# Optimization experiments

Measured on AMD Instinct MI355X. Metric: run time of the kernel, lower is better.

Reference implementation:

```python
import jax, jax.numpy as jnp
import numpy as np

N, NF, DIM, H, DH, DEPTH, EDIM, NB = 256, 127, 128, 8, 64, 6, 3, 512
INNER = H * DH  # 512
SCALE = DH ** -0.5
EPS = 1e-5


def setup_inputs() -> dict:
    key = jax.random.key(0)
    ks = jax.random.split(key, 16)
    p = lambda k, shape: jax.random.normal(k, shape, jnp.float32) * 0.02
    return {
        "coordinates": jax.random.normal(ks[0], (N, 3), jnp.float32),
        "bonds": jax.random.randint(ks[1], (NB, 2), 0, N),
        "noise_level": jax.random.uniform(ks[2], (1,), jnp.float32),
        "atom_emb": p(ks[3], (N, NF)),
        "ln1_g": jnp.ones((DEPTH, DIM)), "ln1_b": jnp.zeros((DEPTH, DIM)),
        "Wq": p(ks[4], (DEPTH, DIM, INNER)), "bq": jnp.zeros((DEPTH, INNER)),
        "Wkv": p(ks[5], (DEPTH, DIM, 2 * INNER)), "bkv": jnp.zeros((DEPTH, 2 * INNER)),
        "We": p(ks[6], (DEPTH, EDIM, INNER)), "be": jnp.zeros((DEPTH, INNER)),
        "Wo": p(ks[7], (DEPTH, INNER, DIM)), "bo": jnp.zeros((DEPTH, DIM)),
        "Wg1": p(ks[8], (DEPTH, 3 * DIM)),
        "ln2_g": jnp.ones((DEPTH, DIM)), "ln2_b": jnp.zeros((DEPTH, DIM)),
        "W1": p(ks[9], (DEPTH, DIM, 4 * DIM)), "b1": jnp.zeros((DEPTH, 4 * DIM)),
        "W2": p(ks[10], (DEPTH, 4 * DIM, DIM)), "b2": jnp.zeros((DEPTH, DIM)),
        "Wg2": p(ks[11], (DEPTH, 3 * DIM)),
        "out_w": p(ks[12], (DIM, 1)), "out_b": jnp.zeros((1,)),
    }


def _layernorm(x, g, b):
    m = jnp.mean(x, axis=-1, keepdims=True)
    v = jnp.mean((x - m) ** 2, axis=-1, keepdims=True)
    return (x - m) * jax.lax.rsqrt(v + EPS) * g + b


def _gated_residual(x, res, Wg):
    # Linear(3*dim -> 1, no bias) then sigmoid; mask is all-True so no masking.
    gate = jax.nn.sigmoid(jnp.concatenate([x, res, x - res], axis=-1) @ Wg)[..., None]
    return x * gate + res * (1.0 - gate)


def _forward(coordinates, bonds, noise_level, atom_emb, ln1_g, ln1_b, Wq, bq,
             Wkv, bkv, We, be, Wo, bo, Wg1, ln2_g, ln2_b, W1, b1, W2, b2, Wg2,
             out_w, out_b):
    n = coordinates.shape[0]
    # nodes: [n, NF] atom embeddings (looked up at arange(n)) + noise column -> [n, DIM]
    noise_col = jnp.broadcast_to(noise_level.reshape(1, 1), (n, 1))
    nodes = jnp.concatenate([atom_emb, noise_col], axis=-1)
    # dense edge tensor [n, n, 3]: coordinate differences at bonded pairs, antisymmetric
    bi, bj = bonds[:, 0], bonds[:, 1]
    diff = coordinates[bi] - coordinates[bj]
    edges = jnp.zeros((n, n, EDIM), jnp.float32).at[bi, bj].set(diff).at[bj, bi].set(-diff)

    for l in range(DEPTH):
        # --- edge-biased multi-head attention (PreNorm) ---
        x = _layernorm(nodes, ln1_g[l], ln1_b[l])
        q = (x @ Wq[l] + bq[l]).reshape(n, H, DH).transpose(1, 0, 2)          # [h, i, d]
        kv = x @ Wkv[l] + bkv[l]
        k = kv[:, :INNER].reshape(n, H, DH).transpose(1, 0, 2)                # [h, j, d]
        v = kv[:, INNER:].reshape(n, H, DH).transpose(1, 0, 2)                # [h, j, d]
        e = (edges @ We[l] + be[l]).reshape(n, n, H, DH).transpose(2, 0, 1, 3)  # [h, i, j, d]
        k_ij = k[:, None, :, :] + e                                            # [h, i, j, d]
        v_ij = v[:, None, :, :] + e
        sim = jnp.einsum('hid,hijd->hij', q, k_ij) * SCALE
        attn = jax.nn.softmax(sim, axis=-1)  # mask is all ones -> no-op
        out = jnp.einsum('hij,hijd->hid', attn, v_ij)                          # [h, i, d]
        out = out.transpose(1, 0, 2).reshape(n, INNER) @ Wo[l] + bo[l]         # [n, DIM]
        nodes = _gated_residual(out, nodes, Wg1[l])
        # --- feedforward (PreNorm) + gated residual ---
        y = _layernorm(nodes, ln2_g[l], ln2_b[l])
        y = jax.nn.gelu(y @ W1[l] + b1[l], approximate=False) @ W2[l] + b2[l]
        nodes = _gated_residual(y, nodes, Wg2[l])

    energy = nodes @ out_w + out_b  # [n, 1]
    return energy[None, :, :]       # [1, n, 1]


def reference(coordinates, bonds, noise_level, atom_emb, ln1_g, ln1_b, Wq, bq,
              Wkv, bkv, We, be, Wo, bo, Wg1, ln2_g, ln2_b, W1, b1, W2, b2, Wg2,
              out_w, out_b):
    return _forward(coordinates, bonds, noise_level, atom_emb, ln1_g, ln1_b,
                    Wq, bq, Wkv, bkv, We, be, Wo, bo, Wg1, ln2_g, ln2_b,
                    W1, b1, W2, b2, Wg2, out_w, out_b)
```

## Files before the change

kernel.cpp:

```cpp
#include <hip/hip_runtime.h>

#define NN     256
#define NF     127
#define DIM    128
#define NH     8
#define DH     64
#define INNER  512
#define DEPTH  6
#define NB     512
#define ATTN_SCALE 0.125f
#define LN_EPS 1e-5f

#define FMA4(A_, S_, V_) { A_.x=fmaf(S_,(V_).x,A_.x); A_.y=fmaf(S_,(V_).y,A_.y); \
                           A_.z=fmaf(S_,(V_).z,A_.z); A_.w=fmaf(S_,(V_).w,A_.w); }

__device__ __forceinline__ float wred_sum(float v){
#pragma unroll
  for(int o=32;o;o>>=1) v += __shfl_xor(v,o);
  return v;
}
__device__ __forceinline__ float wred_max(float v){
#pragma unroll
  for(int o=32;o;o>>=1) v = fmaxf(v,__shfl_xor(v,o));
  return v;
}
__device__ __forceinline__ float2 wred_sum2(float a, float b){
#pragma unroll
  for(int o=32;o;o>>=1){ a += __shfl_xor(a,o); b += __shfl_xor(b,o); }
  return make_float2(a,b);
}

__device__ __forceinline__ void ln_wave(float n0, float n1,
                                        const float* g, const float* b, int l,
                                        float& x0, float& x1){
  float2 sv = wred_sum2(n0+n1, n0*n0+n1*n1);
  float m  = sv.x*(1.f/DIM);
  float var = sv.y*(1.f/DIM) - m*m;
  float rs = rsqrtf(var + LN_EPS);
  x0 = (n0-m)*rs*g[l]    + b[l];
  x1 = (n1-m)*rs*g[64+l] + b[64+l];
}

__device__ __forceinline__ void gate_wave(float o0, float o1, float& n0, float& n1,
                                          const float* Wg, int l){
  float gv = o0*Wg[l]    + n0*Wg[DIM+l]    + (o0-n0)*Wg[2*DIM+l]
           + o1*Wg[64+l] + n1*Wg[DIM+64+l] + (o1-n1)*Wg[2*DIM+64+l];
  gv = wred_sum(gv);
  float gate = 1.f/(1.f + expf(-gv));
  n0 = o0*gate + n0*(1.f-gate);
  n1 = o1*gate + n1*(1.f-gate);
}

__device__ __forceinline__ void mvp128_512(const float* xin, const float* W,
                                           float* SC, int t){
  const int cg4 = (t&127)<<2, fq = t>>7;
  float4 acc = make_float4(0.f,0.f,0.f,0.f);
#pragma unroll 8
  for(int f=fq*32; f<fq*32+32; f++){
    float4 wv = *(const float4*)(W + f*INNER + cg4);
    float xv = xin[f];
    FMA4(acc, xv, wv);
  }
  *(float4*)(SC + fq*INNER + cg4) = acc;
}

__device__ __forceinline__ void mvp128_1024(const float* xin, const float* W,
                                            float* SC, int t){
  const int cg4 = (t&255)<<2, rh = t>>8;
  float4 acc = make_float4(0.f,0.f,0.f,0.f);
#pragma unroll 8
  for(int f=rh*64; f<rh*64+64; f++){
    float4 wv = *(const float4*)(W + f*(2*INNER) + cg4);
    float xv = xin[f];
    FMA4(acc, xv, wv);
  }
  *(float4*)(SC + rh*(2*INNER) + cg4) = acc;
}

__device__ __forceinline__ void mvp512_128(const float* ain, const float* W,
                                           float* SC, int t){
  const int cg4 = (t&31)<<2, fg = t>>5;
  float4 acc = make_float4(0.f,0.f,0.f,0.f);
#pragma unroll 8
  for(int f=fg*32; f<fg*32+32; f++){
    float4 wv = *(const float4*)(W + f*DIM + cg4);
    float av = ain[f];
    FMA4(acc, av, wv);
  }
  *(float4*)(SC + fg*DIM + cg4) = acc;
}

__device__ __forceinline__ void qkv_tail(const float* xs, int i,
    const float* Wq, const float* bq, const float* Wkv, const float* bkv,
    const float* be, float* qgn, float* kTn, float* vgn, float* SC, int t){
  mvp128_512(xs, Wq, SC, t);
  __syncthreads();
  qgn[i*INNER + t] = bq[t] + SC[t] + SC[INNER+t] + SC[2*INNER+t] + SC[3*INNER+t];
  __syncthreads();
  mvp128_1024(xs, Wkv, SC, t);
  __syncthreads();
#pragma unroll
  for(int cc=0; cc<2; cc++){
    int c = t + cc*512;
    float s = bkv[c] + SC[c] + SC[2*INNER+c];
    if(c < INNER) kTn[c*NN + i]            = s + be[c];
    else          vgn[i*INNER + c - INNER] = s + be[c-INNER];
  }
}

__global__ __launch_bounds__(512) void k_qkv0(const float* atom_emb, const float* noise,
    float* nodes, const float* ln1_g, const float* ln1_b,
    const float* Wq, const float* bq, const float* Wkv, const float* bkv, const float* be,
    float* qg, float* kT, float* vg){
  __shared__ __align__(16) float SC[2048];
  __shared__ __align__(16) float xsm[DIM];
  const int t = threadIdx.x, i = blockIdx.x;
  const int w = t>>6, l = t&63;
  float nd0 = (l<NF)?      atom_emb[i*NF + l]      : noise[0];
  float nd1 = (64+l<NF)?   atom_emb[i*NF + 64 + l] : noise[0];
  if(w==0){ nodes[i*DIM + l] = nd0; nodes[i*DIM + 64 + l] = nd1; }
  float x0, x1;
  ln_wave(nd0, nd1, ln1_g, ln1_b, l, x0, x1);
  xsm[l] = x0; xsm[64+l] = x1;
  __syncthreads();
  qkv_tail(xsm, i, Wq, bq, Wkv, bkv, be, qg, kT, vg, SC, t);
}

__global__ __launch_bounds__(512) void k_layer(
    float* nodes, const float* qg, const float* kT, const float* vg,
    float* qg_n, float* kT_n, float* vg_n,
    const int* bonds, const float* coords,
    const float* We,
    const float* Wo, const float* bo, const float* Wg1,
    const float* ln2_g, const float* ln2_b,
    const float* W1, const float* b1, const float* W2, const float* b2,
    const float* Wg2,
    const float* ln1_g_n, const float* ln1_b_n,
    const float* Wq_n, const float* bq_n, const float* Wkv_n, const float* bkv_n,
    const float* be_n,
    const float* out_w, const float* out_b, float* eout, int has_next)
{
  __shared__ __align__(16) float SC[2048];
  __shared__ __align__(16) float qs[INNER];
  __shared__ __align__(16) float ao[INNER];
  __shared__ __align__(16) float eb[3*NN];
  __shared__ __align__(16) float xsm[DIM];
  const int t = threadIdx.x, i = blockIdx.x;
  const int w = t>>6, l = t&63;

  qs[t] = qg[i*INNER + t];
  eb[t&511] = 0.f;
  if(t < 256) eb[512 + t] = 0.f;
  float nd0 = nodes[i*DIM + l];
  float nd1 = nodes[i*DIM + 64 + l];
  __syncthreads();

  {
    const int bi = bonds[2*t], bj = bonds[2*t+1];
    if(bi==i || bj==i){
      float dx = coords[3*bi+0] - coords[3*bj+0];
      float dy = coords[3*bi+1] - coords[3*bj+1];
      float dz = coords[3*bi+2] - coords[3*bj+2];
      if(bi==i){ eb[bj]=dx;  eb[NN+bj]=dy;  eb[2*NN+bj]=dz;  }
      if(bj==i){ eb[bi]=-dx; eb[NN+bi]=-dy; eb[2*NN+bi]=-dz; }
    }
  }
  __syncthreads();

  {
    const int h = w, j0 = l<<2, qb = h*DH;
    float qwe0, qwe1, qwe2;
    {
      float qv = qs[qb + l];
      qwe0 = qv*We[0*INNER + qb + l];
      qwe1 = qv*We[1*INNER + qb + l];
      qwe2 = qv*We[2*INNER + qb + l];
#pragma unroll
      for(int o=32;o;o>>=1){
        qwe0 += __shfl_xor(qwe0,o); qwe1 += __shfl_xor(qwe1,o); qwe2 += __shfl_xor(qwe2,o);
      }
    }
    const float* kTh = kT + qb*NN;
    float s0=0.f,s1=0.f,s2=0.f,s3=0.f;
#pragma unroll 8
    for(int o=0;o<DH;o++){
      float qv = qs[qb + o];
      float4 kk = *(const float4*)(kTh + o*NN + j0);
      s0=fmaf(qv,kk.x,s0); s1=fmaf(qv,kk.y,s1); s2=fmaf(qv,kk.z,s2); s3=fmaf(qv,kk.w,s3);
    }
    float4 ex = *(const float4*)(eb + j0);
    float4 ey = *(const float4*)(eb + NN + j0);
    float4 ez = *(const float4*)(eb + 2*NN + j0);
    s0 = (s0 + qwe0*ex.x + qwe1*ey.x + qwe2*ez.x)*ATTN_SCALE;
    s1 = (s1 + qwe0*ex.y + qwe1*ey.y + qwe2*ez.y)*ATTN_SCALE;
    s2 = (s2 + qwe0*ex.z + qwe1*ey.z + qwe2*ez.z)*ATTN_SCALE;
    s3 = (s3 + qwe0*ex.w + qwe1*ey.w + qwe2*ez.w)*ATTN_SCALE;
    float mx = wred_max(fmaxf(fmaxf(s0,s1),fmaxf(s2,s3)));
    float p0=expf(s0-mx), p1=expf(s1-mx), p2=expf(s2-mx), p3=expf(s3-mx);
    float inv = 1.f / wred_sum(p0+p1+p2+p3);
    float a0=p0*inv, a1=p1*inv, a2=p2*inv, a3=p3*inv;
    *(float4*)(SC + h*NN + j0) = make_float4(a0,a1,a2,a3);
    float c0 = a0*ex.x + a1*ex.y + a2*ex.z + a3*ex.w;
    float c1 = a0*ey.x + a1*ey.y + a2*ey.z + a3*ey.w;
    float c2 = a0*ez.x + a1*ez.y + a2*ez.z + a3*ez.w;
    c0 = wred_sum(c0); c1 = wred_sum(c1); c2 = wred_sum(c2);
    __builtin_amdgcn_wave_barrier();
    const int dq = (l&15)<<2, jg = l>>4;
    const float* vb = vg + qb + dq;
    float4 acc = make_float4(0.f,0.f,0.f,0.f);
#pragma unroll 8
    for(int jj=0;jj<64;jj++){
      int j = (jg<<6) + ((jj + (jg<<3)) & 63);
      float a = SC[h*NN + j];
      float4 vv = *(const float4*)(vb + j*INNER);
      FMA4(acc, a, vv);
    }
#pragma unroll
    for(int o=16;o<64;o<<=1){
      acc.x += __shfl_xor(acc.x,o); acc.y += __shfl_xor(acc.y,o);
      acc.z += __shfl_xor(acc.z,o); acc.w += __shfl_xor(acc.w,o);
    }
    if(l<16){
      float4 we0 = *(const float4*)(We + 0*INNER + qb + dq);
      float4 we1 = *(const float4*)(We + 1*INNER + qb + dq);
      float4 we2 = *(const float4*)(We + 2*INNER + qb + dq);
      float4 ov;
      ov.x = acc.x + c0*we0.x + c1*we1.x + c2*we2.x;
      ov.y = acc.y + c0*we0.y + c1*we1.y + c2*we2.y;
      ov.z = acc.z + c0*we0.z + c1*we1.z + c2*we2.z;
      ov.w = acc.w + c0*we0.w + c1*we1.w + c2*we2.w;
      *(float4*)(ao + qb + dq) = ov;
    }
  }
  __syncthreads();

  mvp512_128(ao, Wo, SC, t);
  __syncthreads();
  {
    float o0 = bo[l], o1 = bo[64+l];
#pragma unroll
    for(int fg=0; fg<16; fg++){ o0 += SC[fg*DIM + l]; o1 += SC[fg*DIM + 64 + l]; }
    gate_wave(o0, o1, nd0, nd1, Wg1, l);
    float x0, x1;
    ln_wave(nd0, nd1, ln2_g, ln2_b, l, x0, x1);
    xsm[l] = x0; xsm[64+l] = x1;
  }
  __syncthreads();

  mvp128_512(xsm, W1, SC, t);
  __syncthreads();
  {
    float a = b1[t] + SC[t] + SC[INNER+t] + SC[2*INNER+t] + SC[3*INNER+t];
    qs[t] = 0.5f*a*(1.f + erff(a*0.70710678118654752440f));
  }
  __syncthreads();
  mvp512_128(qs, W2, SC, t);
  __syncthreads();
  {
    float y0 = b2[l], y1 = b2[64+l];
#pragma unroll
    for(int fg=0; fg<16; fg++){ y0 += SC[fg*DIM + l]; y1 += SC[fg*DIM + 64 + l]; }
    gate_wave(y0, y1, nd0, nd1, Wg2, l);
    if(w==0){ nodes[i*DIM + l] = nd0; nodes[i*DIM + 64 + l] = nd1; }
    if(has_next){
      float x0, x1;
      ln_wave(nd0, nd1, ln1_g_n, ln1_b_n, l, x0, x1);
      xsm[l] = x0; xsm[64+l] = x1;
    } else if(w==0){
      float ev = nd0*out_w[l] + nd1*out_w[64+l];
      ev = wred_sum(ev);
      if(l==0) eout[i] = ev + out_b[0];
    }
  }
  if(has_next){
    __syncthreads();
    qkv_tail(xsm, i, Wq_n, bq_n, Wkv_n, bkv_n, be_n, qg_n, kT_n, vg_n, SC, t);
  }
}

extern "C" void kernel_launch(void* const* d_in, const int* in_sizes, int n_in,
                              void* d_out, int out_size, void* d_ws, size_t ws_size,
                              hipStream_t stream){
  const float* coords   = (const float*)d_in[0];
  const int*   bonds    = (const int*  )d_in[1];
  const float* noise    = (const float*)d_in[2];
  const float* atom_emb = (const float*)d_in[3];
  const float* ln1_g = (const float*)d_in[4];
  const float* ln1_b = (const float*)d_in[5];
  const float* Wq    = (const float*)d_in[6];
  const float* bq    = (const float*)d_in[7];
  const float* Wkv   = (const float*)d_in[8];
  const float* bkv   = (const float*)d_in[9];
  const float* We    = (const float*)d_in[10];
  const float* be    = (const float*)d_in[11];
  const float* Wo    = (const float*)d_in[12];
  const float* bo    = (const float*)d_in[13];
  const float* Wg1   = (const float*)d_in[14];
  const float* ln2_g = (const float*)d_in[15];
  const float* ln2_b = (const float*)d_in[16];
  const float* W1    = (const float*)d_in[17];
  const float* b1    = (const float*)d_in[18];
  const float* W2    = (const float*)d_in[19];
  const float* b2    = (const float*)d_in[20];
  const float* Wg2   = (const float*)d_in[21];
  const float* out_w = (const float*)d_in[22];
  const float* out_b = (const float*)d_in[23];

  float* ws = (float*)d_ws;
  float* nodes   = ws;
  float* qbuf[2] = { ws +  32768, ws + 163840 };
  float* kbuf[2] = { ws + 294912, ws + 425984 };
  float* vbuf[2] = { ws + 557056, ws + 688128 };

  k_qkv0<<<NN, 512, 0, stream>>>(atom_emb, noise, nodes, ln1_g, ln1_b,
                                 Wq, bq, Wkv, bkv, be,
                                 qbuf[0], kbuf[0], vbuf[0]);
  for(int l=0; l<DEPTH; l++){
    int cur = l&1, nxt = cur^1;
    int has_next = (l < DEPTH-1);
    int ln = has_next ? l+1 : l;
    k_layer<<<NN, 512, 0, stream>>>(
      nodes, qbuf[cur], kbuf[cur], vbuf[cur],
      qbuf[nxt], kbuf[nxt], vbuf[nxt],
      bonds, coords,
      We  + (size_t)l*3*INNER,
      Wo  + (size_t)l*INNER*DIM, bo + (size_t)l*DIM, Wg1 + (size_t)l*3*DIM,
      ln2_g + (size_t)l*DIM, ln2_b + (size_t)l*DIM,
      W1  + (size_t)l*DIM*4*DIM, b1 + (size_t)l*4*DIM,
      W2  + (size_t)l*4*DIM*DIM, b2 + (size_t)l*DIM, Wg2 + (size_t)l*3*DIM,
      ln1_g + (size_t)ln*DIM, ln1_b + (size_t)ln*DIM,
      Wq  + (size_t)ln*DIM*INNER, bq + (size_t)ln*INNER,
      Wkv + (size_t)ln*DIM*2*INNER, bkv + (size_t)ln*2*INNER,
      be  + (size_t)ln*INNER,
      out_w, out_b, (float*)d_out, has_next);
  }
}
```

Baseline: 304.9 us.

## Double block size to 1024 threads and split attention across two waves per head

Measured after the change: 322.2 us. +5.7%, slower.

```diff
diff --git a/kernel.cpp b/kernel.cpp
--- a/kernel.cpp
+++ b/kernel.cpp
@@ -8,6 +8,7 @@
 #define INNER  512
 #define DEPTH  6
 #define NB     512
+#define TB     1024
 #define ATTN_SCALE 0.125f
 #define LN_EPS 1e-5f
 
@@ -53,36 +54,34 @@
 
 __device__ __forceinline__ void mvp128_512(const float* xin, const float* W,
                                            float* SC, int t){
-  const int cg4 = (t&127)<<2, fq = t>>7;
+  const int cg4 = (t&127)<<2, fo = t>>7;
   float4 acc = make_float4(0.f,0.f,0.f,0.f);
-#pragma unroll 8
-  for(int f=fq*32; f<fq*32+32; f++){
+#pragma unroll
+  for(int f=fo*16; f<fo*16+16; f++){
     float4 wv = *(const float4*)(W + f*INNER + cg4);
     float xv = xin[f];
     FMA4(acc, xv, wv);
   }
-  *(float4*)(SC + fq*INNER + cg4) = acc;
-}
-
+  *(float4*)(SC + fo*INNER + cg4) = acc;
+}
 __device__ __forceinline__ void mvp128_1024(const float* xin, const float* W,
                                             float* SC, int t){
-  const int cg4 = (t&255)<<2, rh = t>>8;
+  const int cg4 = (t&255)<<2, fq = t>>8;
   float4 acc = make_float4(0.f,0.f,0.f,0.f);
-#pragma unroll 8
-  for(int f=rh*64; f<rh*64+64; f++){
+#pragma unroll
+  for(int f=fq*32; f<fq*32+32; f++){
     float4 wv = *(const float4*)(W + f*(2*INNER) + cg4);
     float xv = xin[f];
     FMA4(acc, xv, wv);
   }
-  *(float4*)(SC + rh*(2*INNER) + cg4) = acc;
-}
-
+  *(float4*)(SC + fq*(2*INNER) + cg4) = acc;
+}
 __device__ __forceinline__ void mvp512_128(const float* ain, const float* W,
                                            float* SC, int t){
   const int cg4 = (t&31)<<2, fg = t>>5;
   float4 acc = make_float4(0.f,0.f,0.f,0.f);
-#pragma unroll 8
-  for(int f=fg*32; f<fg*32+32; f++){
+#pragma unroll
+  for(int f=fg*16; f<fg*16+16; f++){
     float4 wv = *(const float4*)(W + f*DIM + cg4);
     float av = ain[f];
     FMA4(acc, av, wv);
@@ -95,29 +94,35 @@
     const float* be, float* qgn, float* kTn, float* vgn, float* SC, int t){
   mvp128_512(xs, Wq, SC, t);
   __syncthreads();
-  qgn[i*INNER + t] = bq[t] + SC[t] + SC[INNER+t] + SC[2*INNER+t] + SC[3*INNER+t];
+  if(t < INNER){
+    float s = bq[t];
+#pragma unroll
+    for(int fo=0; fo<8; fo++) s += SC[fo*INNER + t];
+    qgn[i*INNER + t] = s;
+  }
   __syncthreads();
   mvp128_1024(xs, Wkv, SC, t);
   __syncthreads();
-#pragma unroll
-  for(int cc=0; cc<2; cc++){
-    int c = t + cc*512;
-    float s = bkv[c] + SC[c] + SC[2*INNER+c];
+  {
+    int c = t;
+    float s = bkv[c];
+#pragma unroll
+    for(int fq=0; fq<4; fq++) s += SC[fq*(2*INNER) + c];
     if(c < INNER) kTn[c*NN + i]            = s + be[c];
     else          vgn[i*INNER + c - INNER] = s + be[c-INNER];
   }
 }
 
-__global__ __launch_bounds__(512) void k_qkv0(const float* atom_emb, const float* noise,
+__global__ __launch_bounds__(TB) void k_qkv0(const float* atom_emb, const float* noise,
     float* nodes, const float* ln1_g, const float* ln1_b,
     const float* Wq, const float* bq, const float* Wkv, const float* bkv, const float* be,
     float* qg, float* kT, float* vg){
-  __shared__ __align__(16) float SC[2048];
+  __shared__ __align__(16) float SC[4096];
   __shared__ __align__(16) float xsm[DIM];
   const int t = threadIdx.x, i = blockIdx.x;
   const int w = t>>6, l = t&63;
-  float nd0 = (l<NF)?      atom_emb[i*NF + l]      : noise[0];
-  float nd1 = (64+l<NF)?   atom_emb[i*NF + 64 + l] : noise[0];
+  float nd0 = (l<NF)?    atom_emb[i*NF + l]      : noise[0];
+  float nd1 = (64+l<NF)? atom_emb[i*NF + 64 + l] : noise[0];
   if(w==0){ nodes[i*DIM + l] = nd0; nodes[i*DIM + 64 + l] = nd1; }
   float x0, x1;
   ln_wave(nd0, nd1, ln1_g, ln1_b, l, x0, x1);
@@ -126,7 +131,7 @@
   qkv_tail(xsm, i, Wq, bq, Wkv, bkv, be, qg, kT, vg, SC, t);
 }
 
-__global__ __launch_bounds__(512) void k_layer(
+__global__ __launch_bounds__(TB) void k_layer(
     float* nodes, const float* qg, const float* kT, const float* vg,
     float* qg_n, float* kT_n, float* vg_n,
     const int* bonds, const float* coords,
@@ -140,22 +145,25 @@
     const float* be_n,
     const float* out_w, const float* out_b, float* eout, int has_next)
 {
-  __shared__ __align__(16) float SC[2048];
+  __shared__ __align__(16) float SC[4096];
+  __shared__ __align__(16) float aW[NH*NN];
+  __shared__ __align__(16) float aoP[2*NH*DH];
+  __shared__ __align__(16) float cEs[NH*3];
   __shared__ __align__(16) float qs[INNER];
   __shared__ __align__(16) float ao[INNER];
   __shared__ __align__(16) float eb[3*NN];
   __shared__ __align__(16) float xsm[DIM];
+  __shared__ __align__(16) float o128[DIM];
   const int t = threadIdx.x, i = blockIdx.x;
   const int w = t>>6, l = t&63;
 
-  qs[t] = qg[i*INNER + t];
-  eb[t&511] = 0.f;
-  if(t < 256) eb[512 + t] = 0.f;
+  if(t < INNER) qs[t] = qg[i*INNER + t];
+  if(t < 3*NN)  eb[t] = 0.f;
   float nd0 = nodes[i*DIM + l];
   float nd1 = nodes[i*DIM + 64 + l];
   __syncthreads();
 
-  {
+  if(t < NB){
     const int bi = bonds[2*t], bj = bonds[2*t+1];
     if(bi==i || bj==i){
       float dx = coords[3*bi+0] - coords[3*bj+0];
@@ -168,7 +176,7 @@
   __syncthreads();
 
   {
-    const int h = w, j0 = l<<2, qb = h*DH;
+    const int h = w>>1, half = w&1, j0 = l<<2, qb = h*DH;
     float qwe0, qwe1, qwe2;
     {
       float qv = qs[qb + l];
@@ -182,36 +190,41 @@
     }
     const float* kTh = kT + qb*NN;
     float s0=0.f,s1=0.f,s2=0.f,s3=0.f;
-#pragma unroll 8
-    for(int o=0;o<DH;o++){
+#pragma unroll
+    for(int o=half*32; o<half*32+32; o++){
       float qv = qs[qb + o];
       float4 kk = *(const float4*)(kTh + o*NN + j0);
       s0=fmaf(qv,kk.x,s0); s1=fmaf(qv,kk.y,s1); s2=fmaf(qv,kk.z,s2); s3=fmaf(qv,kk.w,s3);
     }
+    *(float4*)(SC + (half*NH + h)*NN + j0) = make_float4(s0,s1,s2,s3);
+    __syncthreads();
+    float4 pA = *(const float4*)(SC + h*NN + j0);
+    float4 pB = *(const float4*)(SC + (NH+h)*NN + j0);
     float4 ex = *(const float4*)(eb + j0);
     float4 ey = *(const float4*)(eb + NN + j0);
     float4 ez = *(const float4*)(eb + 2*NN + j0);
-    s0 = (s0 + qwe0*ex.x + qwe1*ey.x + qwe2*ez.x)*ATTN_SCALE;
-    s1 = (s1 + qwe0*ex.y + qwe1*ey.y + qwe2*ez.y)*ATTN_SCALE;
-    s2 = (s2 + qwe0*ex.z + qwe1*ey.z + qwe2*ez.z)*ATTN_SCALE;
-    s3 = (s3 + qwe0*ex.w + qwe1*ey.w + qwe2*ez.w)*ATTN_SCALE;
+    s0 = (pA.x+pB.x + qwe0*ex.x + qwe1*ey.x + qwe2*ez.x)*ATTN_SCALE;
+    s1 = (pA.y+pB.y + qwe0*ex.y + qwe1*ey.y + qwe2*ez.y)*ATTN_SCALE;
+    s2 = (pA.z+pB.z + qwe0*ex.z + qwe1*ey.z + qwe2*ez.z)*ATTN_SCALE;
+    s3 = (pA.w+pB.w + qwe0*ex.w + qwe1*ey.w + qwe2*ez.w)*ATTN_SCALE;
     float mx = wred_max(fmaxf(fmaxf(s0,s1),fmaxf(s2,s3)));
     float p0=expf(s0-mx), p1=expf(s1-mx), p2=expf(s2-mx), p3=expf(s3-mx);
     float inv = 1.f / wred_sum(p0+p1+p2+p3);
     float a0=p0*inv, a1=p1*inv, a2=p2*inv, a3=p3*inv;
-    *(float4*)(SC + h*NN + j0) = make_float4(a0,a1,a2,a3);
+    if(half==0) *(float4*)(aW + h*NN + j0) = make_float4(a0,a1,a2,a3);
     float c0 = a0*ex.x + a1*ex.y + a2*ex.z + a3*ex.w;
     float c1 = a0*ey.x + a1*ey.y + a2*ey.z + a3*ey.w;
     float c2 = a0*ez.x + a1*ez.y + a2*ez.z + a3*ez.w;
     c0 = wred_sum(c0); c1 = wred_sum(c1); c2 = wred_sum(c2);
-    __builtin_amdgcn_wave_barrier();
+    if(half==0 && l==0){ cEs[h*3+0]=c0; cEs[h*3+1]=c1; cEs[h*3+2]=c2; }
+    __syncthreads();
     const int dq = (l&15)<<2, jg = l>>4;
     const float* vb = vg + qb + dq;
     float4 acc = make_float4(0.f,0.f,0.f,0.f);
-#pragma unroll 8
-    for(int jj=0;jj<64;jj++){
-      int j = (jg<<6) + ((jj + (jg<<3)) & 63);
-      float a = SC[h*NN + j];
+#pragma unroll
+    for(int jj=0;jj<32;jj++){
+      int j = half*128 + (jg<<5) + ((jj + (jg<<3)) & 31);
+      float a = aW[h*NN + j];
       float4 vv = *(const float4*)(vb + j*INNER);
       FMA4(acc, a, vv);
     }
@@ -220,26 +233,28 @@
       acc.x += __shfl_xor(acc.x,o); acc.y += __shfl_xor(acc.y,o);
       acc.z += __shfl_xor(acc.z,o); acc.w += __shfl_xor(acc.w,o);
     }
-    if(l<16){
-      float4 we0 = *(const float4*)(We + 0*INNER + qb + dq);
-      float4 we1 = *(const float4*)(We + 1*INNER + qb + dq);
-      float4 we2 = *(const float4*)(We + 2*INNER + qb + dq);
-      float4 ov;
-      ov.x = acc.x + c0*we0.x + c1*we1.x + c2*we2.x;
-      ov.y = acc.y + c0*we0.y + c1*we1.y + c2*we2.y;
-      ov.z = acc.z + c0*we0.z + c1*we1.z + c2*we2.z;
-      ov.w = acc.w + c0*we0.w + c1*we1.w + c2*we2.w;
-      *(float4*)(ao + qb + dq) = ov;
-    }
+    if(l<16) *(float4*)(aoP + (half*NH + h)*DH + dq) = acc;
+  }
+  __syncthreads();
+  if(t < INNER){
+    const int c = t, h2 = c>>6, d = c&63;
+    ao[c] = aoP[h2*DH + d] + aoP[(NH+h2)*DH + d]
+          + cEs[h2*3+0]*We[0*INNER+c] + cEs[h2*3+1]*We[1*INNER+c]
+          + cEs[h2*3+2]*We[2*INNER+c];
   }
   __syncthreads();
 
   mvp512_128(ao, Wo, SC, t);
   __syncthreads();
+  if(t < DIM){
+    float s = bo[t];
+#pragma unroll
+    for(int fg=0; fg<32; fg++) s += SC[fg*DIM + t];
+    o128[t] = s;
+  }
+  __syncthreads();
   {
-    float o0 = bo[l], o1 = bo[64+l];
-#pragma unroll
-    for(int fg=0; fg<16; fg++){ o0 += SC[fg*DIM + l]; o1 += SC[fg*DIM + 64 + l]; }
+    float o0 = o128[l], o1 = o128[64+l];
     gate_wave(o0, o1, nd0, nd1, Wg1, l);
     float x0, x1;
     ln_wave(nd0, nd1, ln2_g, ln2_b, l, x0, x1);
@@ -249,17 +264,24 @@
 
   mvp128_512(xsm, W1, SC, t);
   __syncthreads();
+  if(t < INNER){
+    float a = b1[t];
+#pragma unroll
+    for(int fo=0; fo<8; fo++) a += SC[fo*INNER + t];
+    qs[t] = 0.5f*a*(1.f + erff(a*0.70710678118654752440f));
+  }
+  __syncthreads();
+  mvp512_128(qs, W2, SC, t);
+  __syncthreads();
+  if(t < DIM){
+    float s = b2[t];
+#pragma unroll
+    for(int fg=0; fg<32; fg++) s += SC[fg*DIM + t];
+    o128[t] = s;
+  }
+  __syncthreads();
   {
-    float a = b1[t] + SC[t] + SC[INNER+t] + SC[2*INNER+t] + SC[3*INNER+t];
-    qs[t] = 0.5f*a*(1.f + erff(a*0.70710678118654752440f));
-  }
-  __syncthreads();
-  mvp512_128(qs, W2, SC, t);
-  __syncthreads();
-  {
-    float y0 = b2[l], y1 = b2[64+l];
-#pragma unroll
-    for(int fg=0; fg<16; fg++){ y0 += SC[fg*DIM + l]; y1 += SC[fg*DIM + 64 + l]; }
+    float y0 = o128[l], y1 = o128[64+l];
     gate_wave(y0, y1, nd0, nd1, Wg2, l);
     if(w==0){ nodes[i*DIM + l] = nd0; nodes[i*DIM + 64 + l] = nd1; }
     if(has_next){
@@ -274,7 +296,8 @@
   }
   if(has_next){
     __syncthreads();
-    qkv_tail(xsm, i, Wq_n, bq_n, Wkv_n, bkv_n, be_n, qg_n, kT_n, vg_n, SC, t);
+    qkv_tail(xsm, i, Wq_n, bq_n, Wkv_n, bkv_n, be_n,
+             qg_n, kT_n, vg_n, SC, t);
   }
 }
 
@@ -312,14 +335,14 @@
   float* kbuf[2] = { ws + 294912, ws + 425984 };
   float* vbuf[2] = { ws + 557056, ws + 688128 };
 
-  k_qkv0<<<NN, 512, 0, stream>>>(atom_emb, noise, nodes, ln1_g, ln1_b,
-                                 Wq, bq, Wkv, bkv, be,
-                                 qbuf[0], kbuf[0], vbuf[0]);
+  k_qkv0<<<NN, TB, 0, stream>>>(atom_emb, noise, nodes, ln1_g, ln1_b,
+                                Wq, bq, Wkv, bkv, be,
+                                qbuf[0], kbuf[0], vbuf[0]);
   for(int l=0; l<DEPTH; l++){
     int cur = l&1, nxt = cur^1;
     int has_next = (l < DEPTH-1);
     int ln = has_next ? l+1 : l;
-    k_layer<<<NN, 512, 0, stream>>>(
+    k_layer<<<NN, TB, 0, stream>>>(
       nodes, qbuf[cur], kbuf[cur], vbuf[cur],
       qbuf[nxt], kbuf[nxt], vbuf[nxt],
       bonds, coords,
```

## Split attention into separate head-major kernel grouping eight queries per block

Applied to the files above, without the earlier changes.

Result: no change. 303.6 us (-0.4%).

```diff
diff --git a/kernel.cpp b/kernel.cpp
--- a/kernel.cpp
+++ b/kernel.cpp
@@ -63,7 +63,6 @@
   }
   *(float4*)(SC + fq*INNER + cg4) = acc;
 }
-
 __device__ __forceinline__ void mvp128_1024(const float* xin, const float* W,
                                             float* SC, int t){
   const int cg4 = (t&255)<<2, rh = t>>8;
@@ -76,7 +75,6 @@
   }
   *(float4*)(SC + rh*(2*INNER) + cg4) = acc;
 }
-
 __device__ __forceinline__ void mvp512_128(const float* ain, const float* W,
                                            float* SC, int t){
   const int cg4 = (t&31)<<2, fg = t>>5;
@@ -116,8 +114,8 @@
   __shared__ __align__(16) float xsm[DIM];
   const int t = threadIdx.x, i = blockIdx.x;
   const int w = t>>6, l = t&63;
-  float nd0 = (l<NF)?      atom_emb[i*NF + l]      : noise[0];
-  float nd1 = (64+l<NF)?   atom_emb[i*NF + 64 + l] : noise[0];
+  float nd0 = (l<NF)?    atom_emb[i*NF + l]      : noise[0];
+  float nd1 = (64+l<NF)? atom_emb[i*NF + 64 + l] : noise[0];
   if(w==0){ nodes[i*DIM + l] = nd0; nodes[i*DIM + 64 + l] = nd1; }
   float x0, x1;
   ln_wave(nd0, nd1, ln1_g, ln1_b, l, x0, x1);
@@ -126,11 +124,105 @@
   qkv_tail(xsm, i, Wq, bq, Wkv, bkv, be, qg, kT, vg, SC, t);
 }
 
+__global__ __launch_bounds__(512) void k_attn(
+    const float* qg, const float* kT, const float* vg,
+    const int* bonds, const float* coords, const float* We,
+    float* aog)
+{
+  __shared__ __align__(16) float qsm[8*DH];
+  __shared__ __align__(16) float eb[8][3*NN];
+  __shared__ __align__(16) float aW[8][NN];
+  const int t = threadIdx.x;
+  const int h = blockIdx.x >> 5, i0 = (blockIdx.x & 31) << 3;
+  const int w = t>>6, l = t&63;
+  const int qb = h*DH, j0 = l<<2;
+
+  qsm[w*DH + l] = qg[(i0+w)*INNER + qb + l];
+#pragma unroll
+  for(int cc=0; cc<12; cc++) (&eb[0][0])[cc*512 + t] = 0.f;
+  __syncthreads();
+
+  {
+    const int bi = bonds[2*t], bj = bonds[2*t+1];
+    const bool hi = (bi>=i0 && bi<i0+8), hj = (bj>=i0 && bj<i0+8);
+    if(hi || hj){
+      float dx = coords[3*bi+0] - coords[3*bj+0];
+      float dy = coords[3*bi+1] - coords[3*bj+1];
+      float dz = coords[3*bi+2] - coords[3*bj+2];
+      if(hi){ float* e = eb[bi-i0]; e[bj]=dx;  e[NN+bj]=dy;  e[2*NN+bj]=dz;  }
+      if(hj){ float* e = eb[bj-i0]; e[bi]=-dx; e[NN+bi]=-dy; e[2*NN+bi]=-dz; }
+    }
+  }
+  __syncthreads();
+
+  float qwe0, qwe1, qwe2;
+  {
+    float qv = qsm[w*DH + l];
+    qwe0 = qv*We[0*INNER + qb + l];
+    qwe1 = qv*We[1*INNER + qb + l];
+    qwe2 = qv*We[2*INNER + qb + l];
+#pragma unroll
+    for(int o=32;o;o>>=1){
+      qwe0 += __shfl_xor(qwe0,o); qwe1 += __shfl_xor(qwe1,o); qwe2 += __shfl_xor(qwe2,o);
+    }
+  }
+  const float* kTh = kT + qb*NN;
+  float s0=0.f,s1=0.f,s2=0.f,s3=0.f;
+#pragma unroll 8
+  for(int o=0;o<DH;o++){
+    float qv = qsm[w*DH + o];
+    float4 kk = *(const float4*)(kTh + o*NN + j0);
+    s0=fmaf(qv,kk.x,s0); s1=fmaf(qv,kk.y,s1); s2=fmaf(qv,kk.z,s2); s3=fmaf(qv,kk.w,s3);
+  }
+  const float* e = eb[w];
+  float4 ex = *(const float4*)(e + j0);
+  float4 ey = *(const float4*)(e + NN + j0);
+  float4 ez = *(const float4*)(e + 2*NN + j0);
+  s0 = (s0 + qwe0*ex.x + qwe1*ey.x + qwe2*ez.x)*ATTN_SCALE;
+  s1 = (s1 + qwe0*ex.y + qwe1*ey.y + qwe2*ez.y)*ATTN_SCALE;
+  s2 = (s2 + qwe0*ex.z + qwe1*ey.z + qwe2*ez.z)*ATTN_SCALE;
+  s3 = (s3 + qwe0*ex.w + qwe1*ey.w + qwe2*ez.w)*ATTN_SCALE;
+  float mx = wred_max(fmaxf(fmaxf(s0,s1),fmaxf(s2,s3)));
+  float p0=expf(s0-mx), p1=expf(s1-mx), p2=expf(s2-mx), p3=expf(s3-mx);
+  float inv = 1.f / wred_sum(p0+p1+p2+p3);
+  float a0=p0*inv, a1=p1*inv, a2=p2*inv, a3=p3*inv;
+  *(float4*)(aW[w] + j0) = make_float4(a0,a1,a2,a3);
+  float c0 = a0*ex.x + a1*ex.y + a2*ex.z + a3*ex.w;
+  float c1 = a0*ey.x + a1*ey.y + a2*ey.z + a3*ey.w;
+  float c2 = a0*ez.x + a1*ez.y + a2*ez.z + a3*ez.w;
+  c0 = wred_sum(c0); c1 = wred_sum(c1); c2 = wred_sum(c2);
+  __builtin_amdgcn_wave_barrier();
+  const int dq = (l&15)<<2, jg = l>>4;
+  const float* vb = vg + qb + dq;
+  float4 acc = make_float4(0.f,0.f,0.f,0.f);
+#pragma unroll 8
+  for(int jj=0;jj<64;jj++){
+    int j = (jg<<6) + ((jj + (jg<<3)) & 63);
+    float a = aW[w][j];
+    float4 vv = *(const float4*)(vb + j*INNER);
+    FMA4(acc, a, vv);
+  }
+#pragma unroll
+  for(int o=16;o<64;o<<=1){
+    acc.x += __shfl_xor(acc.x,o); acc.y += __shfl_xor(acc.y,o);
+    acc.z += __shfl_xor(acc.z,o); acc.w += __shfl_xor(acc.w,o);
+  }
+  if(l<16){
+    float4 we0 = *(const float4*)(We + 0*INNER + qb + dq);
+    float4 we1 = *(const float4*)(We + 1*INNER + qb + dq);
+    float4 we2 = *(const float4*)(We + 2*INNER + qb + dq);
+    float4 ov;
+    ov.x = acc.x + c0*we0.x + c1*we1.x + c2*we2.x;
+    ov.y = acc.y + c0*we0.y + c1*we1.y + c2*we2.y;
+    ov.z = acc.z + c0*we0.z + c1*we1.z + c2*we2.z;
+    ov.w = acc.w + c0*we0.w + c1*we1.w + c2*we2.w;
+    *(float4*)(aog + (i0+w)*INNER + qb + dq) = ov;
+  }
+}
+
 __global__ __launch_bounds__(512) void k_layer(
-    float* nodes, const float* qg, const float* kT, const float* vg,
+    float* nodes, const float* aog,
     float* qg_n, float* kT_n, float* vg_n,
-    const int* bonds, const float* coords,
-    const float* We,
     const float* Wo, const float* bo, const float* Wg1,
     const float* ln2_g, const float* ln2_b,
     const float* W1, const float* b1, const float* W2, const float* b2,
@@ -142,99 +234,17 @@
 {
   __shared__ __align__(16) float SC[2048];
   __shared__ __align__(16) float qs[INNER];
-  __shared__ __align__(16) float ao[INNER];
-  __shared__ __align__(16) float eb[3*NN];
+  __shared__ __align__(16) float aos[INNER];
   __shared__ __align__(16) float xsm[DIM];
   const int t = threadIdx.x, i = blockIdx.x;
   const int w = t>>6, l = t&63;
 
-  qs[t] = qg[i*INNER + t];
-  eb[t&511] = 0.f;
-  if(t < 256) eb[512 + t] = 0.f;
+  aos[t] = aog[i*INNER + t];
   float nd0 = nodes[i*DIM + l];
   float nd1 = nodes[i*DIM + 64 + l];
   __syncthreads();
 
-  {
-    const int bi = bonds[2*t], bj = bonds[2*t+1];
-    if(bi==i || bj==i){
-      float dx = coords[3*bi+0] - coords[3*bj+0];
-      float dy = coords[3*bi+1] - coords[3*bj+1];
-      float dz = coords[3*bi+2] - coords[3*bj+2];
-      if(bi==i){ eb[bj]=dx;  eb[NN+bj]=dy;  eb[2*NN+bj]=dz;  }
-      if(bj==i){ eb[bi]=-dx; eb[NN+bi]=-dy; eb[2*NN+bi]=-dz; }
-    }
-  }
-  __syncthreads();
-
-  {
-    const int h = w, j0 = l<<2, qb = h*DH;
-    float qwe0, qwe1, qwe2;
-    {
-      float qv = qs[qb + l];
-      qwe0 = qv*We[0*INNER + qb + l];
-      qwe1 = qv*We[1*INNER + qb + l];
-      qwe2 = qv*We[2*INNER + qb + l];
-#pragma unroll
-      for(int o=32;o;o>>=1){
-        qwe0 += __shfl_xor(qwe0,o); qwe1 += __shfl_xor(qwe1,o); qwe2 += __shfl_xor(qwe2,o);
-      }
-    }
-    const float* kTh = kT + qb*NN;
-    float s0=0.f,s1=0.f,s2=0.f,s3=0.f;
-#pragma unroll 8
-    for(int o=0;o<DH;o++){
-      float qv = qs[qb + o];
-      float4 kk = *(const float4*)(kTh + o*NN + j0);
-      s0=fmaf(qv,kk.x,s0); s1=fmaf(qv,kk.y,s1); s2=fmaf(qv,kk.z,s2); s3=fmaf(qv,kk.w,s3);
-    }
-    float4 ex = *(const float4*)(eb + j0);
-    float4 ey = *(const float4*)(eb + NN + j0);
-    float4 ez = *(const float4*)(eb + 2*NN + j0);
-    s0 = (s0 + qwe0*ex.x + qwe1*ey.x + qwe2*ez.x)*ATTN_SCALE;
-    s1 = (s1 + qwe0*ex.y + qwe1*ey.y + qwe2*ez.y)*ATTN_SCALE;
-    s2 = (s2 + qwe0*ex.z + qwe1*ey.z + qwe2*ez.z)*ATTN_SCALE;
-    s3 = (s3 + qwe0*ex.w + qwe1*ey.w + qwe2*ez.w)*ATTN_SCALE;
-    float mx = wred_max(fmaxf(fmaxf(s0,s1),fmaxf(s2,s3)));
-    float p0=expf(s0-mx), p1=expf(s1-mx), p2=expf(s2-mx), p3=expf(s3-mx);
-    float inv = 1.f / wred_sum(p0+p1+p2+p3);
-    float a0=p0*inv, a1=p1*inv, a2=p2*inv, a3=p3*inv;
-    *(float4*)(SC + h*NN + j0) = make_float4(a0,a1,a2,a3);
-    float c0 = a0*ex.x + a1*ex.y + a2*ex.z + a3*ex.w;
-    float c1 = a0*ey.x + a1*ey.y + a2*ey.z + a3*ey.w;
-    float c2 = a0*ez.x + a1*ez.y + a2*ez.z + a3*ez.w;
-    c0 = wred_sum(c0); c1 = wred_sum(c1); c2 = wred_sum(c2);
-    __builtin_amdgcn_wave_barrier();
-    const int dq = (l&15)<<2, jg = l>>4;
-    const float* vb = vg + qb + dq;
-    float4 acc = make_float4(0.f,0.f,0.f,0.f);
-#pragma unroll 8
-    for(int jj=0;jj<64;jj++){
-      int j = (jg<<6) + ((jj + (jg<<3)) & 63);
-      float a = SC[h*NN + j];
-      float4 vv = *(const float4*)(vb + j*INNER);
-      FMA4(acc, a, vv);
-    }
-#pragma unroll
-    for(int o=16;o<64;o<<=1){
-      acc.x += __shfl_xor(acc.x,o); acc.y += __shfl_xor(acc.y,o);
-      acc.z += __shfl_xor(acc.z,o); acc.w += __shfl_xor(acc.w,o);
-    }
-    if(l<16){
-      float4 we0 = *(const float4*)(We + 0*INNER + qb + dq);
-      float4 we1 = *(const float4*)(We + 1*INNER + qb + dq);
-      float4 we2 = *(const float4*)(We + 2*INNER + qb + dq);
-      float4 ov;
-      ov.x = acc.x + c0*we0.x + c1*we1.x + c2*we2.x;
-      ov.y = acc.y + c0*we0.y + c1*we1.y + c2*we2.y;
-      ov.z = acc.z + c0*we0.z + c1*we1.z + c2*we2.z;
-      ov.w = acc.w + c0*we0.w + c1*we1.w + c2*we2.w;
-      *(float4*)(ao + qb + dq) = ov;
-    }
-  }
-  __syncthreads();
-
-  mvp512_128(ao, Wo, SC, t);
+  mvp512_128(aos, Wo, SC, t);
   __syncthreads();
   {
     float o0 = bo[l], o1 = bo[64+l];
@@ -274,7 +284,8 @@
   }
   if(has_next){
     __syncthreads();
-    qkv_tail(xsm, i, Wq_n, bq_n, Wkv_n, bkv_n, be_n, qg_n, kT_n, vg_n, SC, t);
+    qkv_tail(xsm, i, Wq_n, bq_n, Wkv_n, bkv_n, be_n,
+             qg_n, kT_n, vg_n, SC, t);
   }
 }
 
@@ -311,6 +322,7 @@
   float* qbuf[2] = { ws +  32768, ws + 163840 };
   float* kbuf[2] = { ws + 294912, ws + 425984 };
   float* vbuf[2] = { ws + 557056, ws + 688128 };
+  float* aobuf   = ws + 819200;
 
   k_qkv0<<<NN, 512, 0, stream>>>(atom_emb, noise, nodes, ln1_g, ln1_b,
                                  Wq, bq, Wkv, bkv, be,
@@ -319,11 +331,12 @@
     int cur = l&1, nxt = cur^1;
     int has_next = (l < DEPTH-1);
     int ln = has_next ? l+1 : l;
+    k_attn<<<NN, 512, 0, stream>>>(
+      qbuf[cur], kbuf[cur], vbuf[cur], bonds, coords,
+      We + (size_t)l*3*INNER, aobuf);
     k_layer<<<NN, 512, 0, stream>>>(
-      nodes, qbuf[cur], kbuf[cur], vbuf[cur],
+      nodes, aobuf,
       qbuf[nxt], kbuf[nxt], vbuf[nxt],
-      bonds, coords,
-      We  + (size_t)l*3*INNER,
       Wo  + (size_t)l*INNER*DIM, bo + (size_t)l*DIM, Wg1 + (size_t)l*3*DIM,
       ln2_g + (size_t)l*DIM, ln2_b + (size_t)l*DIM,
       W1  + (size_t)l*DIM*4*DIM, b1 + (size_t)l*4*DIM,
```
